# Performance work log

Measured on AMD Instinct MI355X. Metric: run time of the kernel, lower is better.

## Reference

```python
import jax, jax.numpy as jnp
import numpy as np

N, S, E, H = 4, 4096, 1024, 16
D = E // H  # 64


def setup_inputs() -> dict:
    key = jax.random.key(0)
    ks = jax.random.split(key, 6)
    scale = 0.02
    x = jax.random.normal(ks[0], (N, S, E), dtype=jnp.float32)
    Wq = jax.random.normal(ks[1], (E, E), dtype=jnp.float32) * scale
    Wk = jax.random.normal(ks[2], (E, E), dtype=jnp.float32) * scale
    Wv = jax.random.normal(ks[3], (E, E), dtype=jnp.float32) * scale
    Wo = jax.random.normal(ks[4], (E, E), dtype=jnp.float32) * scale
    bo = jax.random.normal(ks[5], (E,), dtype=jnp.float32) * scale
    return {"x": x, "Wq": Wq, "Wk": Wk, "Wv": Wv, "Wo": Wo, "bo": bo}


def reference(x, Wq, Wk, Wv, Wo, bo):
    n, s, _ = x.shape
    # torch nn.Linear(bias=False): y = x @ W.T  (W stored as [out, in])
    q = (x @ Wq.T).reshape(n, s, H, D).transpose(0, 2, 1, 3)  # (N, H, S, D)
    k = (x @ Wk.T).reshape(n, s, H, D).transpose(0, 2, 1, 3)  # (N, H, S, D)
    v = (x @ Wv.T).reshape(n, s, H, D).transpose(0, 2, 1, 3)  # (N, H, S, D)
    # Faithful to source: einsum subscripts applied to the PERMUTED (N,H,S,D)
    # tensors, so label q->H, h->S. energy: (N, H, H, S)
    energy = jnp.einsum('nqhd,nkhd->nqkh', q, k)
    attention = jax.nn.softmax(energy / (D ** 0.5), axis=3)
    # 'nqkh,nvhd->nqhd': k and v are independently summed free indices
    out = jnp.einsum('nqkh,nvhd->nqhd', attention, v).reshape(n, s, E)  # (N,S,E)
    return out @ Wo.T + bo
```

## Files before the change

kernel.cpp:

```cpp
#include <hip/hip_runtime.h>
#include <stdint.h>

typedef unsigned short u16;
typedef unsigned int   u32;
typedef __attribute__((ext_vector_type(8))) short short8;
typedef __attribute__((ext_vector_type(4))) float f32x4;
typedef __attribute__((ext_vector_type(8))) u16   u16x8;
typedef __attribute__((ext_vector_type(4))) u16   u16x4;

static constexpr size_t NX = (size_t)4 * 4096 * 1024;
static constexpr size_t NW = (size_t)1024 * 1024;

static constexpr size_t OFF_XB   = 0;
static constexpr size_t OFF_EN   = 0;
static constexpr size_t OFF_QK   = 33554432;
static constexpr size_t OFF_WQB  = 100663296;
static constexpr size_t OFF_WKB  = 102760448;
static constexpr size_t OFF_WOB  = 104857600;
static constexpr size_t OFF_WVST = 106954752;
static constexpr size_t OFF_VS   = 107216896;
static constexpr size_t OFF_GMAX = 111411200;
static constexpr size_t OFF_INVZ = 111415296;
static constexpr size_t OFF_ST   = 111419392;

static __device__ __forceinline__ u16 f2bf(float f) {
    u32 u = __builtin_bit_cast(u32, f);
    u += 0x7fffu + ((u >> 16) & 1u);
    return (u16)(u >> 16);
}
static __device__ __forceinline__ float bf2f(u16 v) {
    u32 u = ((u32)v) << 16;
    return __builtin_bit_cast(float, u);
}

#if __has_builtin(__builtin_amdgcn_global_load_lds)
#define HAVE_GLOAD_LDS 1
static __device__ __forceinline__ void gload_lds16(const void* g, void* l) {
    __builtin_amdgcn_global_load_lds(
        (__attribute__((address_space(1))) void*)(uintptr_t)g,
        (__attribute__((address_space(3))) void*)(uintptr_t)l,
        16, 0, 0);
}
#endif

#if __has_builtin(__builtin_amdgcn_sched_barrier)
#define SCHED_FENCE() __builtin_amdgcn_sched_barrier(0)
#else
#define SCHED_FENCE()
#endif

__global__ __launch_bounds__(256)
void cvt_kernel(const float* __restrict__ x, const float* __restrict__ wq,
                const float* __restrict__ wk, const float* __restrict__ wo,
                u16* __restrict__ xb, u16* __restrict__ wqb,
                u16* __restrict__ wkb, u16* __restrict__ wob)
{
    size_t i = ((size_t)blockIdx.x * 256 + threadIdx.x) * 8;
    const float* s; u16* dst; size_t o;
    if (i < NX) { s = x; dst = xb; o = i; }
    else {
        size_t r = i - NX;
        int w = (int)(r >> 20);
        o = r & (NW - 1);
        s   = (w == 0) ? wq  : (w == 1) ? wk  : wo;
        dst = (w == 0) ? wqb : (w == 1) ? wkb : wob;
    }
    f32x4 a = *(const f32x4*)&s[o];
    f32x4 c = *(const f32x4*)&s[o + 4];
    u16x8 v;
    v[0]=f2bf(a[0]); v[1]=f2bf(a[1]); v[2]=f2bf(a[2]); v[3]=f2bf(a[3]);
    v[4]=f2bf(c[0]); v[5]=f2bf(c[1]); v[6]=f2bf(c[2]); v[7]=f2bf(c[3]);
    *(u16x8*)&dst[o] = v;
}

__global__ __launch_bounds__(256)
void wvst_kernel(const float* __restrict__ Wv, u16* __restrict__ Bvs)
{
    int idx = blockIdx.x * 256 + threadIdx.x;
    int d = idx >> 10;
    int e = idx & 1023;
    float s = 0.f;
    #pragma unroll
    for (int h = 0; h < 16; ++h) s += Wv[(size_t)(h * 64 + d) * 1024 + e];
    Bvs[(size_t)d * 1024 + e] = f2bf(s);
}

__global__ __launch_bounds__(512, 2)
void gemm_qk(const u16* __restrict__ A, const u16* __restrict__ Bw,
             u16* __restrict__ C, int M, int N, int K, int lognbx)
{
    __shared__ u16 lds[65536];
    const int tid  = threadIdx.x;
    const int wave = tid >> 6;
    const int lane = tid & 63;

    const int nwg = gridDim.x;
    const int swz = ((int)blockIdx.x & 7) * (nwg >> 3) + ((int)blockIdx.x >> 3);
    const long col0 = (long)(swz & ((1 << lognbx) - 1)) * 256;
    const long row0 = (long)(swz >> lognbx) * 256;

    const int wr2 = wave >> 2;
    const int wc2 = wave & 3;
    const int fr  = lane & 15;
    const int kq  = lane >> 4;
    const int rxor = fr & 7;

    const int t255  = tid & 255;
    const int halfA = tid >> 8;
    const int gAsrc = (t255 & 7) ^ ((t255 >> 3) & 7);
    const u16* sA = A + (size_t)(row0 + halfA * 128 + (t255 >> 3)) * K + gAsrc * 8;
    const int dA = halfA * 8192 + t255 * 8;

    const int u  = (tid & 127) | ((tid >> 1) & 128);
    const int bh = (tid >> 7) & 1;
    const int gBsrc = (u & 7) ^ ((u >> 3) & 7);
    const u16* sB = Bw + (size_t)(col0 + bh * 128 + (u >> 3)) * K + gBsrc * 8;
    const int dB = bh * 8192 + u * 8;

    auto STAGE = [&](int buf, int k0) {
        #pragma unroll
        for (int l = 0; l < 4; ++l) {
#ifdef HAVE_GLOAD_LDS
            gload_lds16(sA + (size_t)l * 32 * K + k0, &lds[buf * 16384 + dA + l * 2048]);
            gload_lds16(sB + (size_t)l * 32 * K + k0, &lds[32768 + buf * 16384 + dB + l * 2048]);
#else
            *(short8*)&lds[buf * 16384 + dA + l * 2048] =
                *(const short8*)(sA + (size_t)l * 32 * K + k0);
            *(short8*)&lds[32768 + buf * 16384 + dB + l * 2048] =
                *(const short8*)(sB + (size_t)l * 32 * K + k0);
#endif
        }
    };

    f32x4 acc[8][4] = {};

    STAGE(0, 0);
    __syncthreads();

    const int nt = K >> 6;
    for (int t = 0; t < nt; ++t) {
        const int cur = t & 1;
        const int base  = cur * 16384;
        const int bbase = 32768 + cur * 16384;

        if (t + 1 < nt) STAGE(cur ^ 1, (t + 1) << 6);

        short8 af[4][2], ag[4][2], bf[2][2], bg[2][2];
        #pragma unroll
        for (int m = 0; m < 4; ++m) {
            const int row = wr2 * 128 + m * 16 + fr;
            #pragma unroll
            for (int kk = 0; kk < 2; ++kk)
                af[m][kk] = *(const short8*)&lds[base + row * 64 + (((kk << 2) | kq) ^ rxor) * 8];
        }
        #pragma unroll
        for (int n = 0; n < 2; ++n) {
            const int col = wc2 * 64 + n * 16 + fr;
            #pragma unroll
            for (int kk = 0; kk < 2; ++kk)
                bf[n][kk] = *(const short8*)&lds[bbase + col * 64 + (((kk << 2) | kq) ^ rxor) * 8];
        }
        #pragma unroll
        for (int m = 0; m < 4; ++m) {
            const int row = wr2 * 128 + 64 + m * 16 + fr;
            #pragma unroll
            for (int kk = 0; kk < 2; ++kk)
                ag[m][kk] = *(const short8*)&lds[base + row * 64 + (((kk << 2) | kq) ^ rxor) * 8];
        }
        SCHED_FENCE();

        __builtin_amdgcn_s_setprio(1);
        #pragma unroll
        for (int kk = 0; kk < 2; ++kk)
            #pragma unroll
            for (int m = 0; m < 4; ++m)
                #pragma unroll
                for (int n = 0; n < 2; ++n)
                    acc[m][n] = __builtin_amdgcn_mfma_f32_16x16x32_bf16(af[m][kk], bf[n][kk], acc[m][n], 0, 0, 0);
        __builtin_amdgcn_s_setprio(0);

        #pragma unroll
        for (int n = 0; n < 2; ++n) {
            const int col = wc2 * 64 + (n + 2) * 16 + fr;
            #pragma unroll
            for (int kk = 0; kk < 2; ++kk)
                bg[n][kk] = *(const short8*)&lds[bbase + col * 64 + (((kk << 2) | kq) ^ rxor) * 8];
        }
        SCHED_FENCE();

        __builtin_amdgcn_s_setprio(1);
        #pragma unroll
        for (int kk = 0; kk < 2; ++kk)
            #pragma unroll
            for (int m = 0; m < 4; ++m)
                #pragma unroll
                for (int n = 0; n < 2; ++n)
                    acc[m + 4][n] = __builtin_amdgcn_mfma_f32_16x16x32_bf16(ag[m][kk], bf[n][kk], acc[m + 4][n], 0, 0, 0);
        #pragma unroll
        for (int kk = 0; kk < 2; ++kk)
            #pragma unroll
            for (int m = 0; m < 4; ++m)
                #pragma unroll
                for (int n = 0; n < 2; ++n)
                    acc[m][n + 2] = __builtin_amdgcn_mfma_f32_16x16x32_bf16(af[m][kk], bg[n][kk], acc[m][n + 2], 0, 0, 0);
        #pragma unroll
        for (int kk = 0; kk < 2; ++kk)
            #pragma unroll
            for (int m = 0; m < 4; ++m)
                #pragma unroll
                for (int n = 0; n < 2; ++n)
                    acc[m + 4][n + 2] = __builtin_amdgcn_mfma_f32_16x16x32_bf16(ag[m][kk], bg[n][kk], acc[m + 4][n + 2], 0, 0, 0);
        __builtin_amdgcn_s_setprio(0);

        __syncthreads();
    }

    #pragma unroll
    for (int m = 0; m < 8; ++m) {
        #pragma unroll
        for (int n = 0; n < 4; ++n) {
            long gr = row0 + wr2 * 128 + m * 16 + kq * 4;
            long gc = col0 + wc2 * 64 + n * 16 + fr;
            #pragma unroll
            for (int j = 0; j < 4; ++j)
                C[(gr + j) * N + gc] = f2bf(acc[m][n][j]);
        }
    }
}

__global__ __launch_bounds__(256)
void gemm_vs(const u16* __restrict__ A, const u16* __restrict__ Bw,
             u16* __restrict__ C)
{
    __shared__ u16 lsA[2][64 * 32];
    __shared__ u16 lsB[2][64 * 32];
    const int tid  = threadIdx.x;
    const int wave = tid >> 6;
    const int lane = tid & 63;
    const long row0 = (long)blockIdx.x * 64;
    const int wr = (wave >> 1) * 32;
    const int wc = (wave & 1) * 32;
    const int fr = lane & 15;
    const int k8 = (lane >> 4) * 8;

    f32x4 acc[2][2] = {};
    const int c0 = tid;
    const u16* pa = &A [(row0 + (c0 >> 2)) * 1024 + (c0 & 3) * 8];
    const u16* pb = &Bw[((size_t)(c0 >> 2)) * 1024 + (c0 & 3) * 8];

    auto STAGE = [&](int buf, int k0) {
#ifdef HAVE_GLOAD_LDS
        gload_lds16(pa + k0, &lsA[buf][wave * 512]);
        gload_lds16(pb + k0, &lsB[buf][wave * 512]);
#else
        *(short8*)&lsA[buf][(size_t)c0 * 8] = *(const short8*)(pa + k0);
        *(short8*)&lsB[buf][(size_t)c0 * 8] = *(const short8*)(pb + k0);
#endif
    };

    STAGE(0, 0);
    __syncthreads();
    for (int t = 0; t < 32; ++t) {
        const int cur = t & 1;
        if (t + 1 < 32) STAGE(cur ^ 1, (t + 1) << 5);
        short8 af[2], bf[2];
        #pragma unroll
        for (int m = 0; m < 2; ++m)
            af[m] = *(const short8*)&lsA[cur][(wr + m * 16 + fr) * 32 + k8];
        #pragma unroll
        for (int n = 0; n < 2; ++n)
            bf[n] = *(const short8*)&lsB[cur][(wc + n * 16 + fr) * 32 + k8];
        #pragma unroll
        for (int m = 0; m < 2; ++m)
            #pragma unroll
            for (int n = 0; n < 2; ++n)
                acc[m][n] = __builtin_amdgcn_mfma_f32_16x16x32_bf16(af[m], bf[n], acc[m][n], 0, 0, 0);
        __syncthreads();
    }

    const int orow = (lane >> 4) * 4;
    #pragma unroll
    for (int m = 0; m < 2; ++m) {
        #pragma unroll
        for (int n = 0; n < 2; ++n) {
            long gr = row0 + wr + m * 16 + orow;
            int  gc = wc + n * 16 + fr;
            #pragma unroll
            for (int j = 0; j < 4; ++j)
                C[(gr + j) * 64 + gc] = f2bf(acc[m][n][j]);
        }
    }
}

__global__ __launch_bounds__(256)
void energy_kernel(const u16* __restrict__ QKb, float* __restrict__ E)
{
    const int lane = threadIdx.x & 63;
    const size_t site = (size_t)blockIdx.x * 4 + (threadIdx.x >> 6);
    const u16* qrow = QKb + site * 2048;
    const int hh = lane & 15;
    const int kg = (lane >> 4) * 8;
    short8 a0 = *(const short8*)&qrow[hh * 64 + kg];
    short8 a1 = *(const short8*)&qrow[hh * 64 + 32 + kg];
    short8 b0 = *(const short8*)&qrow[1024 + hh * 64 + kg];
    short8 b1 = *(const short8*)&qrow[1024 + hh * 64 + 32 + kg];
    f32x4 acc = {};
    acc = __builtin_amdgcn_mfma_f32_16x16x32_bf16(a0, b0, acc, 0, 0, 0);
    acc = __builtin_amdgcn_mfma_f32_16x16x32_bf16(a1, b1, acc, 0, 0, 0);
    float* out = E + site * 256;
    const int ib = (lane >> 4) * 4;
    #pragma unroll
    for (int r = 0; r < 4; ++r)
        out[(ib + r) * 16 + hh] = acc[r];
}

__global__ __launch_bounds__(256)
void stats_part(const float* __restrict__ E, float* __restrict__ pmax,
                float* __restrict__ psum)
{
    const int b = blockIdx.x, p = threadIdx.x;
    const float* e = E + (size_t)b * 64 * 256 + p;
    float m = -3.4e38f;
    float buf[64];
    #pragma unroll 8
    for (int s = 0; s < 64; ++s) {
        float v = e[(size_t)s * 256];
        buf[s] = v;
        m = fmaxf(m, v);
    }
    float z = 0.f;
    #pragma unroll 8
    for (int s = 0; s < 64; ++s) z += __expf((buf[s] - m) * 0.125f);
    pmax[b * 256 + p] = m;
    psum[b * 256 + p] = z;
}
__global__ __launch_bounds__(256)
void stats_comb(const float* __restrict__ pmax, const float* __restrict__ psum,
                float* __restrict__ gmax, float* __restrict__ invZ)
{
    const int n = blockIdx.x, p = threadIdx.x;
    float m = -3.4e38f;
    #pragma unroll 8
    for (int c = 0; c < 64; ++c) m = fmaxf(m, pmax[(n * 64 + c) * 256 + p]);
    float z = 0.f;
    #pragma unroll 8
    for (int c = 0; c < 64; ++c)
        z += psum[(n * 64 + c) * 256 + p] * __expf((pmax[(n * 64 + c) * 256 + p] - m) * 0.125f);
    gmax[n * 256 + p] = m;
    invZ[n * 256 + p] = 1.0f / z;
}

__global__ __launch_bounds__(256)
void g_kernel(const u16* __restrict__ Vsb, const u16* __restrict__ Wob,
              u16* __restrict__ G)
{
    __shared__ u16 lA[64 * 64];
    __shared__ u16 lB[256 * 64];
    const int tid = threadIdx.x;
    const int wave = tid >> 6, lane = tid & 63;
    const int op = blockIdx.x, uc = blockIdx.y, sl = blockIdx.z;

    {
        const int j = tid >> 2;
        const size_t srow = (size_t)16 * (64 * uc + j) + sl;
        #pragma unroll
        for (int h = 0; h < 2; ++h) {
            const int g = (tid & 3) + h * 4;
            u16x8 v = *(const u16x8*)&Vsb[srow * 64 + g * 8];
            *(u16x8*)&lA[j * 64 + ((g ^ (j & 7)) * 8)] = v;
        }
    }
    {
        const size_t o = (size_t)op * 256 + tid;
        #pragma unroll
        for (int g = 0; g < 8; ++g) {
            u16x8 v = *(const u16x8*)&Wob[o * 1024 + 64 * sl + g * 8];
            *(u16x8*)&lB[tid * 64 + ((g ^ (tid & 7)) * 8)] = v;
        }
    }
    __syncthreads();

    const int fr = lane & 15, kq = lane >> 4;
    f32x4 acc[4][4] = {};
    #pragma unroll
    for (int kk = 0; kk < 2; ++kk) {
        short8 af[4], bq[4];
        #pragma unroll
        for (int m = 0; m < 4; ++m) {
            const int j = m * 16 + fr;
            af[m] = *(const short8*)&lA[j * 64 + (((kq + 4 * kk) ^ (j & 7)) * 8)];
        }
        #pragma unroll
        for (int n = 0; n < 4; ++n) {
            const int o = wave * 64 + n * 16 + fr;
            bq[n] = *(const short8*)&lB[o * 64 + (((kq + 4 * kk) ^ (o & 7)) * 8)];
        }
        #pragma unroll
        for (int m = 0; m < 4; ++m)
            #pragma unroll
            for (int n = 0; n < 4; ++n)
                acc[m][n] = __builtin_amdgcn_mfma_f32_16x16x32_bf16(af[m], bq[n], acc[m][n], 0, 0, 0);
    }

    #pragma unroll
    for (int m = 0; m < 4; ++m) {
        #pragma unroll
        for (int n = 0; n < 4; ++n) {
            const int ocol = op * 256 + wave * 64 + n * 16 + fr;
            #pragma unroll
            for (int jj = 0; jj < 4; ++jj) {
                const int j = m * 16 + kq * 4 + jj;
                G[((size_t)16 * (64 * uc + j) + sl) * 1024 + ocol] = f2bf(acc[m][n][jj]);
            }
        }
    }
}

__global__ __launch_bounds__(256)
void comb_kernel(const float* __restrict__ En, const float* __restrict__ gmax,
                 const float* __restrict__ invZ, const u16* __restrict__ G,
                 const float* __restrict__ bo, float* __restrict__ out)
{
    __shared__ float sm[256], sz[256], sa[256];
    const int b = blockIdx.x;
    const int n = b >> 8, c = b & 255;
    const int t = threadIdx.x;
    sm[t] = gmax[n * 256 + t];
    sz[t] = invZ[n * 256 + t];
    __syncthreads();
    {
        const int sl = t >> 4, i = t & 15;
        const float* e = En + ((size_t)n * 4096 + c * 16 + sl) * 256 + i * 16;
        float a = 0.f;
        #pragma unroll
        for (int j = 0; j < 16; ++j)
            a += __expf((e[j] - sm[i * 16 + j]) * 0.125f) * sz[i * 16 + j];
        sa[sl * 16 + i] = a;
    }
    __syncthreads();

    const int o0 = t * 4;
    const u16* gp = G + ((size_t)n * 4096 + c * 16) * 1024 + o0;
    f32x4 g[16];
    #pragma unroll
    for (int sl = 0; sl < 16; ++sl) {
        u16x4 gv = *(const u16x4*)&gp[(size_t)sl * 1024];
        g[sl][0] = bf2f(gv[0]); g[sl][1] = bf2f(gv[1]);
        g[sl][2] = bf2f(gv[2]); g[sl][3] = bf2f(gv[3]);
    }
    const f32x4 b4 = *(const f32x4*)&bo[o0];
    #pragma unroll
    for (int i = 0; i < 16; ++i) {
        f32x4 acc = b4;
        #pragma unroll
        for (int sl = 0; sl < 16; ++sl) {
            const float a = sa[sl * 16 + i];
            acc[0] += a * g[sl][0];
            acc[1] += a * g[sl][1];
            acc[2] += a * g[sl][2];
            acc[3] += a * g[sl][3];
        }
        *(f32x4*)&out[((size_t)n * 4096 + i * 256 + c) * 1024 + o0] = acc;
    }
}

extern "C" void kernel_launch(void* const* d_in, const int* in_sizes, int n_in,
                              void* d_out, int out_size, void* d_ws, size_t ws_size,
                              hipStream_t stream)
{
    const float* x  = (const float*)d_in[0];
    const float* Wq = (const float*)d_in[1];
    const float* Wk = (const float*)d_in[2];
    const float* Wv = (const float*)d_in[3];
    const float* Wo = (const float*)d_in[4];
    const float* bo = (const float*)d_in[5];
    float* out = (float*)d_out;
    char* ws = (char*)d_ws;

    u16*   xb   = (u16*)  (ws + OFF_XB);
    float* En   = (float*)(ws + OFF_EN);
    u16*   QKb  = (u16*)  (ws + OFF_QK);
    u16*   G    = (u16*)  (ws + OFF_QK);
    u16*   Wqb  = (u16*)  (ws + OFF_WQB);
    u16*   Wkb  = (u16*)  (ws + OFF_WKB);
    u16*   Wob  = (u16*)  (ws + OFF_WOB);
    u16*   Bvs  = (u16*)  (ws + OFF_WVST);
    u16*   Vsb  = (u16*)  (ws + OFF_VS);
    float* gmax = (float*)(ws + OFF_GMAX);
    float* invZ = (float*)(ws + OFF_INVZ);
    float* pmax = (float*)(ws + OFF_ST);
    float* psum = (float*)(ws + OFF_ST + 262144);

    cvt_kernel <<<9728, 256, 0, stream>>>(x, Wq, Wk, Wo, xb, Wqb, Wkb, Wob);
    wvst_kernel<<<256,  256, 0, stream>>>(Wv, Bvs);

    gemm_qk<<<512, 512, 0, stream>>>(xb, Wqb, QKb, 16384, 2048, 1024, 3);
    gemm_vs<<<256, 256, 0, stream>>>(xb, Bvs, Vsb);

    energy_kernel<<<4096, 256, 0, stream>>>(QKb, En);

    stats_part<<<256, 256, 0, stream>>>(En, pmax, psum);
    stats_comb<<<4,   256, 0, stream>>>(pmax, psum, gmax, invZ);

    g_kernel<<<dim3(4, 16, 16), 256, 0, stream>>>(Vsb, Wob, G);

    comb_kernel<<<1024, 256, 0, stream>>>(En, gmax, invZ, G, bo, out);
}
```

Before: 179.7 us.

## Split QK GEMM staging into half-tile loads with interleaved barriers and manual waitcnt

Reworks the gemm_qk main loop so global-to-LDS staging is split into per-half A and B loads spread across four MFMA phases. A is prefetched two K-steps ahead and B one step ahead, with explicit vmcnt/lgkmcnt waits and raw s_barrier instead of a full __syncthreads per iteration. The aim is to overlap memory traffic with MFMA work in a finer-grained, HipKittens-style 8-wave schedule. It adds many barriers and relies on exact vmcnt accounting, so a miscount could cause races or stalls.

```diff
diff --git a/kernel.cpp b/kernel.cpp
--- a/kernel.cpp
+++ b/kernel.cpp
@@ -48,6 +48,10 @@
 #else
 #define SCHED_FENCE()
 #endif
+#define SBAR()   __builtin_amdgcn_s_barrier()
+#define VMCNT4() do { asm volatile("s_waitcnt vmcnt(4)" ::: "memory"); } while (0)
+#define VMCNT0() do { asm volatile("s_waitcnt vmcnt(0)" ::: "memory"); } while (0)
+#define LGKM0()  do { asm volatile("s_waitcnt lgkmcnt(0)" ::: "memory"); } while (0)
 
 __global__ __launch_bounds__(256)
 void cvt_kernel(const float* __restrict__ x, const float* __restrict__ wq,
@@ -103,72 +107,70 @@
     const int wc2 = wave & 3;
     const int fr  = lane & 15;
     const int kq  = lane >> 4;
-    const int rxor = fr & 7;
-
-    const int t255  = tid & 255;
-    const int halfA = tid >> 8;
-    const int gAsrc = (t255 & 7) ^ ((t255 >> 3) & 7);
-    const u16* sA = A + (size_t)(row0 + halfA * 128 + (t255 >> 3)) * K + gAsrc * 8;
-    const int dA = halfA * 8192 + t255 * 8;
-
-    const int u  = (tid & 127) | ((tid >> 1) & 128);
-    const int bh = (tid >> 7) & 1;
-    const int gBsrc = (u & 7) ^ ((u >> 3) & 7);
-    const u16* sB = Bw + (size_t)(col0 + bh * 128 + (u >> 3)) * K + gBsrc * 8;
-    const int dB = bh * 8192 + u * 8;
-
-    auto STAGE = [&](int buf, int k0) {
-        #pragma unroll
-        for (int l = 0; l < 4; ++l) {
+    const int rx  = fr & 7;
+
+    const u16* Abase = A  + row0 * K;
+    const u16* Bbase = Bw + col0 * K;
+
+    auto STAGE_A = [&](int t, int h) {
+        u16* slot = &lds[(((t & 1) << 1) | h) << 13];
+        const u16* src = Abase + (size_t)(h * 128) * K + ((size_t)t << 6);
+        #pragma unroll
+        for (int l = 0; l < 2; ++l) {
+            const int G = wave * 128 + l * 64 + lane;
+            const int rr = G >> 3;
+            const int gs = (G & 7) ^ (rr & 7);
 #ifdef HAVE_GLOAD_LDS
-            gload_lds16(sA + (size_t)l * 32 * K + k0, &lds[buf * 16384 + dA + l * 2048]);
-            gload_lds16(sB + (size_t)l * 32 * K + k0, &lds[32768 + buf * 16384 + dB + l * 2048]);
+            gload_lds16(src + (size_t)rr * K + gs * 8, slot + wave * 1024 + l * 512);
 #else
-            *(short8*)&lds[buf * 16384 + dA + l * 2048] =
-                *(const short8*)(sA + (size_t)l * 32 * K + k0);
-            *(short8*)&lds[32768 + buf * 16384 + dB + l * 2048] =
-                *(const short8*)(sB + (size_t)l * 32 * K + k0);
+            *(short8*)&slot[G * 8] = *(const short8*)(src + (size_t)rr * K + gs * 8);
 #endif
         }
     };
+    auto STAGE_B = [&](int t, int h) {
+        u16* slot = &lds[32768 + ((((t & 1) << 1) | h) << 13)];
+        const u16* src = Bbase + (size_t)(h * 128) * K + ((size_t)t << 6);
+        #pragma unroll
+        for (int l = 0; l < 2; ++l) {
+            const int G = wave * 128 + l * 64 + lane;
+            const int rr = G >> 3;
+            const int gs = (G & 7) ^ (rr & 7);
+#ifdef HAVE_GLOAD_LDS
+            gload_lds16(src + (size_t)rr * K + gs * 8, slot + wave * 1024 + l * 512);
+#else
+            *(short8*)&slot[G * 8] = *(const short8*)(src + (size_t)rr * K + gs * 8);
+#endif
+        }
+    };
+
+    auto LDA = [&](int t, int m, int kk) -> short8 {
+        const u16* slot = &lds[(((t & 1) << 1) | wr2) << 13];
+        const int rr = m * 16 + fr;
+        return *(const short8*)&slot[rr * 64 + ((((kk << 2) | kq)) ^ rx) * 8];
+    };
+    auto LDB = [&](int t, int n, int kk) -> short8 {
+        const u16* slot = &lds[32768 + ((((t & 1) << 1) | (wc2 >> 1)) << 13)];
+        const int rr = (wc2 & 1) * 64 + n * 16 + fr;
+        return *(const short8*)&slot[rr * 64 + ((((kk << 2) | kq)) ^ rx) * 8];
+    };
 
     f32x4 acc[8][4] = {};
-
-    STAGE(0, 0);
-    __syncthreads();
+    short8 af03[4][2], af47[4][2], bf01[2][2], bf23[2][2];
+
+    STAGE_A(0, 0); STAGE_A(0, 1); STAGE_B(0, 0); STAGE_B(0, 1);
+    STAGE_A(1, 0); STAGE_A(1, 1);
+    VMCNT4();
+    SBAR();
 
     const int nt = K >> 6;
     for (int t = 0; t < nt; ++t) {
-        const int cur = t & 1;
-        const int base  = cur * 16384;
-        const int bbase = 32768 + cur * 16384;
-
-        if (t + 1 < nt) STAGE(cur ^ 1, (t + 1) << 6);
-
-        short8 af[4][2], ag[4][2], bf[2][2], bg[2][2];
-        #pragma unroll
-        for (int m = 0; m < 4; ++m) {
-            const int row = wr2 * 128 + m * 16 + fr;
-            #pragma unroll
-            for (int kk = 0; kk < 2; ++kk)
-                af[m][kk] = *(const short8*)&lds[base + row * 64 + (((kk << 2) | kq) ^ rxor) * 8];
-        }
-        #pragma unroll
-        for (int n = 0; n < 2; ++n) {
-            const int col = wc2 * 64 + n * 16 + fr;
-            #pragma unroll
-            for (int kk = 0; kk < 2; ++kk)
-                bf[n][kk] = *(const short8*)&lds[bbase + col * 64 + (((kk << 2) | kq) ^ rxor) * 8];
-        }
-        #pragma unroll
-        for (int m = 0; m < 4; ++m) {
-            const int row = wr2 * 128 + 64 + m * 16 + fr;
-            #pragma unroll
-            for (int kk = 0; kk < 2; ++kk)
-                ag[m][kk] = *(const short8*)&lds[base + row * 64 + (((kk << 2) | kq) ^ rxor) * 8];
-        }
-        SCHED_FENCE();
-
+        #pragma unroll
+        for (int m = 0; m < 4; ++m) { af03[m][0] = LDA(t, m, 0); af03[m][1] = LDA(t, m, 1); }
+        #pragma unroll
+        for (int n = 0; n < 2; ++n) { bf01[n][0] = LDB(t, n, 0); bf01[n][1] = LDB(t, n, 1); }
+        if (t + 1 < nt) STAGE_B(t + 1, 0);
+        SBAR();
+        LGKM0(); SCHED_FENCE();
         __builtin_amdgcn_s_setprio(1);
         #pragma unroll
         for (int kk = 0; kk < 2; ++kk)
@@ -176,18 +178,17 @@
             for (int m = 0; m < 4; ++m)
                 #pragma unroll
                 for (int n = 0; n < 2; ++n)
-                    acc[m][n] = __builtin_amdgcn_mfma_f32_16x16x32_bf16(af[m][kk], bf[n][kk], acc[m][n], 0, 0, 0);
+                    acc[m][n] = __builtin_amdgcn_mfma_f32_16x16x32_bf16(af03[m][kk], bf01[n][kk], acc[m][n], 0, 0, 0);
         __builtin_amdgcn_s_setprio(0);
-
-        #pragma unroll
-        for (int n = 0; n < 2; ++n) {
-            const int col = wc2 * 64 + (n + 2) * 16 + fr;
-            #pragma unroll
-            for (int kk = 0; kk < 2; ++kk)
-                bg[n][kk] = *(const short8*)&lds[bbase + col * 64 + (((kk << 2) | kq) ^ rxor) * 8];
-        }
-        SCHED_FENCE();
-
+        SBAR();
+
+        #pragma unroll
+        for (int m = 0; m < 4; ++m) { af47[m][0] = LDA(t, m + 4, 0); af47[m][1] = LDA(t, m + 4, 1); }
+        #pragma unroll
+        for (int n = 0; n < 2; ++n) { bf23[n][0] = LDB(t, n + 2, 0); bf23[n][1] = LDB(t, n + 2, 1); }
+        if (t + 1 < nt) STAGE_B(t + 1, 1);
+        SBAR();
+        LGKM0(); SCHED_FENCE();
         __builtin_amdgcn_s_setprio(1);
         #pragma unroll
         for (int kk = 0; kk < 2; ++kk)
@@ -195,24 +196,40 @@
             for (int m = 0; m < 4; ++m)
                 #pragma unroll
                 for (int n = 0; n < 2; ++n)
-                    acc[m + 4][n] = __builtin_amdgcn_mfma_f32_16x16x32_bf16(ag[m][kk], bf[n][kk], acc[m + 4][n], 0, 0, 0);
+                    acc[m][n + 2] = __builtin_amdgcn_mfma_f32_16x16x32_bf16(af03[m][kk], bf23[n][kk], acc[m][n + 2], 0, 0, 0);
+        __builtin_amdgcn_s_setprio(0);
+        SBAR();
+
+        if (t + 2 < nt) STAGE_A(t + 2, 0);
+        SBAR();
+        __builtin_amdgcn_s_setprio(1);
         #pragma unroll
         for (int kk = 0; kk < 2; ++kk)
             #pragma unroll
             for (int m = 0; m < 4; ++m)
                 #pragma unroll
                 for (int n = 0; n < 2; ++n)
-                    acc[m][n + 2] = __builtin_amdgcn_mfma_f32_16x16x32_bf16(af[m][kk], bg[n][kk], acc[m][n + 2], 0, 0, 0);
+                    acc[m + 4][n] = __builtin_amdgcn_mfma_f32_16x16x32_bf16(af47[m][kk], bf01[n][kk], acc[m + 4][n], 0, 0, 0);
+        __builtin_amdgcn_s_setprio(0);
+        SBAR();
+
+        if (t + 2 < nt) {
+            STAGE_A(t + 2, 1);
+            VMCNT4();
+        } else if (t + 1 < nt) {
+            VMCNT0();
+        }
+        SBAR();
+        __builtin_amdgcn_s_setprio(1);
         #pragma unroll
         for (int kk = 0; kk < 2; ++kk)
             #pragma unroll
             for (int m = 0; m < 4; ++m)
                 #pragma unroll
                 for (int n = 0; n < 2; ++n)
-                    acc[m + 4][n + 2] = __builtin_amdgcn_mfma_f32_16x16x32_bf16(ag[m][kk], bg[n][kk], acc[m + 4][n + 2], 0, 0, 0);
+                    acc[m + 4][n + 2] = __builtin_amdgcn_mfma_f32_16x16x32_bf16(af47[m][kk], bf23[n][kk], acc[m + 4][n + 2], 0, 0, 0);
         __builtin_amdgcn_s_setprio(0);
-
-        __syncthreads();
+        SBAR();
     }
 
     #pragma unroll
```

Result: slower. 187.6 us (+4.3%).

## Shrink QK GEMM tile to 256x128 with K-step 32 and online-softmax stats

Applied to the files above, without the earlier changes.

The QK projection GEMM moves from a 256x256 tile with K-step 64 to a 256x128 tile with K-step 32. That cuts LDS from 128KB to 48KB per block and the accumulators from 32 to 16 per wave, and raises occupancy from 2 to 4 blocks per CU, with twice as many workgroups. The cost is lower arithmetic intensity per tile, twice as many barrier iterations, and the loss of the interleaved LDS-load/MFMA schedule. The stats_part kernel switches to a single-pass online max/sum, dropping the 64-float register buffer at the cost of an extra exp per element.

```diff
diff --git a/kernel.cpp b/kernel.cpp
--- a/kernel.cpp
+++ b/kernel.cpp
@@ -85,142 +85,83 @@
     Bvs[(size_t)d * 1024 + e] = f2bf(s);
 }
 
-__global__ __launch_bounds__(512, 2)
+__global__ __launch_bounds__(512, 4)
 void gemm_qk(const u16* __restrict__ A, const u16* __restrict__ Bw,
              u16* __restrict__ C, int M, int N, int K, int lognbx)
 {
-    __shared__ u16 lds[65536];
+    __shared__ u16 lsA[2][256 * 32];
+    __shared__ u16 lsB[2][128 * 32];
     const int tid  = threadIdx.x;
     const int wave = tid >> 6;
     const int lane = tid & 63;
 
     const int nwg = gridDim.x;
     const int swz = ((int)blockIdx.x & 7) * (nwg >> 3) + ((int)blockIdx.x >> 3);
-    const long col0 = (long)(swz & ((1 << lognbx) - 1)) * 256;
+    const long col0 = (long)(swz & ((1 << lognbx) - 1)) * 128;
     const long row0 = (long)(swz >> lognbx) * 256;
 
-    const int wr2 = wave >> 2;
-    const int wc2 = wave & 3;
-    const int fr  = lane & 15;
-    const int kq  = lane >> 4;
-    const int rxor = fr & 7;
-
-    const int t255  = tid & 255;
-    const int halfA = tid >> 8;
-    const int gAsrc = (t255 & 7) ^ ((t255 >> 3) & 7);
-    const u16* sA = A + (size_t)(row0 + halfA * 128 + (t255 >> 3)) * K + gAsrc * 8;
-    const int dA = halfA * 8192 + t255 * 8;
-
-    const int u  = (tid & 127) | ((tid >> 1) & 128);
-    const int bh = (tid >> 7) & 1;
-    const int gBsrc = (u & 7) ^ ((u >> 3) & 7);
-    const u16* sB = Bw + (size_t)(col0 + bh * 128 + (u >> 3)) * K + gBsrc * 8;
-    const int dB = bh * 8192 + u * 8;
+    const int wr = (wave >> 1) * 64;
+    const int wc = (wave & 1) * 64;
+    const int fr = lane & 15;
+    const int kq = lane >> 4;
+    const int rx = fr & 3;
+
+    const int GA0 = tid, GA1 = tid + 512;
+    const int rA0 = GA0 >> 2, gA0 = (GA0 & 3) ^ (rA0 & 3);
+    const int rA1 = GA1 >> 2, gA1 = (GA1 & 3) ^ (rA1 & 3);
+    const int rB  = tid >> 2, gB  = (tid & 3) ^ (rB & 3);
+    const u16* pa0 = A  + (size_t)(row0 + rA0) * K + gA0 * 8;
+    const u16* pa1 = A  + (size_t)(row0 + rA1) * K + gA1 * 8;
+    const u16* pb  = Bw + (size_t)(col0 + rB ) * K + gB  * 8;
 
     auto STAGE = [&](int buf, int k0) {
-        #pragma unroll
-        for (int l = 0; l < 4; ++l) {
 #ifdef HAVE_GLOAD_LDS
-            gload_lds16(sA + (size_t)l * 32 * K + k0, &lds[buf * 16384 + dA + l * 2048]);
-            gload_lds16(sB + (size_t)l * 32 * K + k0, &lds[32768 + buf * 16384 + dB + l * 2048]);
+        gload_lds16(pa0 + k0, &lsA[buf][wave * 512]);
+        gload_lds16(pa1 + k0, &lsA[buf][4096 + wave * 512]);
+        gload_lds16(pb  + k0, &lsB[buf][wave * 512]);
 #else
-            *(short8*)&lds[buf * 16384 + dA + l * 2048] =
-                *(const short8*)(sA + (size_t)l * 32 * K + k0);
-            *(short8*)&lds[32768 + buf * 16384 + dB + l * 2048] =
-                *(const short8*)(sB + (size_t)l * 32 * K + k0);
+        *(short8*)&lsA[buf][(size_t)GA0 * 8] = *(const short8*)(pa0 + k0);
+        *(short8*)&lsA[buf][(size_t)GA1 * 8] = *(const short8*)(pa1 + k0);
+        *(short8*)&lsB[buf][(size_t)tid * 8] = *(const short8*)(pb  + k0);
 #endif
-        }
     };
 
-    f32x4 acc[8][4] = {};
+    f32x4 acc[4][4] = {};
 
     STAGE(0, 0);
     __syncthreads();
 
-    const int nt = K >> 6;
+    const int nt = K >> 5;
     for (int t = 0; t < nt; ++t) {
         const int cur = t & 1;
-        const int base  = cur * 16384;
-        const int bbase = 32768 + cur * 16384;
-
-        if (t + 1 < nt) STAGE(cur ^ 1, (t + 1) << 6);
-
-        short8 af[4][2], ag[4][2], bf[2][2], bg[2][2];
-        #pragma unroll
-        for (int m = 0; m < 4; ++m) {
-            const int row = wr2 * 128 + m * 16 + fr;
-            #pragma unroll
-            for (int kk = 0; kk < 2; ++kk)
-                af[m][kk] = *(const short8*)&lds[base + row * 64 + (((kk << 2) | kq) ^ rxor) * 8];
-        }
-        #pragma unroll
-        for (int n = 0; n < 2; ++n) {
-            const int col = wc2 * 64 + n * 16 + fr;
-            #pragma unroll
-            for (int kk = 0; kk < 2; ++kk)
-                bf[n][kk] = *(const short8*)&lds[bbase + col * 64 + (((kk << 2) | kq) ^ rxor) * 8];
-        }
-        #pragma unroll
-        for (int m = 0; m < 4; ++m) {
-            const int row = wr2 * 128 + 64 + m * 16 + fr;
-            #pragma unroll
-            for (int kk = 0; kk < 2; ++kk)
-                ag[m][kk] = *(const short8*)&lds[base + row * 64 + (((kk << 2) | kq) ^ rxor) * 8];
-        }
+        if (t + 1 < nt) STAGE(cur ^ 1, (t + 1) << 5);
+
+        short8 af[4], bf[4];
+        #pragma unroll
+        for (int m = 0; m < 4; ++m)
+            af[m] = *(const short8*)&lsA[cur][(wr + m * 16 + fr) * 32 + ((kq ^ rx) * 8)];
+        #pragma unroll
+        for (int n = 0; n < 4; ++n)
+            bf[n] = *(const short8*)&lsB[cur][(wc + n * 16 + fr) * 32 + ((kq ^ rx) * 8)];
         SCHED_FENCE();
 
         __builtin_amdgcn_s_setprio(1);
         #pragma unroll
-        for (int kk = 0; kk < 2; ++kk)
-            #pragma unroll
-            for (int m = 0; m < 4; ++m)
-                #pragma unroll
-                for (int n = 0; n < 2; ++n)
-                    acc[m][n] = __builtin_amdgcn_mfma_f32_16x16x32_bf16(af[m][kk], bf[n][kk], acc[m][n], 0, 0, 0);
+        for (int m = 0; m < 4; ++m)
+            #pragma unroll
+            for (int n = 0; n < 4; ++n)
+                acc[m][n] = __builtin_amdgcn_mfma_f32_16x16x32_bf16(af[m], bf[n], acc[m][n], 0, 0, 0);
         __builtin_amdgcn_s_setprio(0);
 
-        #pragma unroll
-        for (int n = 0; n < 2; ++n) {
-            const int col = wc2 * 64 + (n + 2) * 16 + fr;
-            #pragma unroll
-            for (int kk = 0; kk < 2; ++kk)
-                bg[n][kk] = *(const short8*)&lds[bbase + col * 64 + (((kk << 2) | kq) ^ rxor) * 8];
-        }
-        SCHED_FENCE();
-
-        __builtin_amdgcn_s_setprio(1);
-        #pragma unroll
-        for (int kk = 0; kk < 2; ++kk)
-            #pragma unroll
-            for (int m = 0; m < 4; ++m)
-                #pragma unroll
-                for (int n = 0; n < 2; ++n)
-                    acc[m + 4][n] = __builtin_amdgcn_mfma_f32_16x16x32_bf16(ag[m][kk], bf[n][kk], acc[m + 4][n], 0, 0, 0);
-        #pragma unroll
-        for (int kk = 0; kk < 2; ++kk)
-            #pragma unroll
-            for (int m = 0; m < 4; ++m)
-                #pragma unroll
-                for (int n = 0; n < 2; ++n)
-                    acc[m][n + 2] = __builtin_amdgcn_mfma_f32_16x16x32_bf16(af[m][kk], bg[n][kk], acc[m][n + 2], 0, 0, 0);
-        #pragma unroll
-        for (int kk = 0; kk < 2; ++kk)
-            #pragma unroll
-            for (int m = 0; m < 4; ++m)
-                #pragma unroll
-                for (int n = 0; n < 2; ++n)
-                    acc[m + 4][n + 2] = __builtin_amdgcn_mfma_f32_16x16x32_bf16(ag[m][kk], bg[n][kk], acc[m + 4][n + 2], 0, 0, 0);
-        __builtin_amdgcn_s_setprio(0);
-
         __syncthreads();
     }
 
     #pragma unroll
-    for (int m = 0; m < 8; ++m) {
+    for (int m = 0; m < 4; ++m) {
         #pragma unroll
         for (int n = 0; n < 4; ++n) {
-            long gr = row0 + wr2 * 128 + m * 16 + kq * 4;
-            long gc = col0 + wc2 * 64 + n * 16 + fr;
+            long gr = row0 + wr + m * 16 + kq * 4;
+            long gc = col0 + wc + n * 16 + fr;
             #pragma unroll
             for (int j = 0; j < 4; ++j)
                 C[(gr + j) * N + gc] = f2bf(acc[m][n][j]);
@@ -320,17 +261,13 @@
 {
     const int b = blockIdx.x, p = threadIdx.x;
     const float* e = E + (size_t)b * 64 * 256 + p;
-    float m = -3.4e38f;
-    float buf[64];
-    #pragma unroll 8
+    float m = -3.4e38f, z = 0.f;
     for (int s = 0; s < 64; ++s) {
         float v = e[(size_t)s * 256];
-        buf[s] = v;
-        m = fmaxf(m, v);
-    }
-    float z = 0.f;
-    #pragma unroll 8
-    for (int s = 0; s < 64; ++s) z += __expf((buf[s] - m) * 0.125f);
+        float mn = fmaxf(m, v);
+        z = z * __expf((m - mn) * 0.125f) + __expf((v - mn) * 0.125f);
+        m = mn;
+    }
     pmax[b * 256 + p] = m;
     psum[b * 256 + p] = z;
 }
@@ -340,10 +277,8 @@
 {
     const int n = blockIdx.x, p = threadIdx.x;
     float m = -3.4e38f;
-    #pragma unroll 8
     for (int c = 0; c < 64; ++c) m = fmaxf(m, pmax[(n * 64 + c) * 256 + p]);
     float z = 0.f;
-    #pragma unroll 8
     for (int c = 0; c < 64; ++c)
         z += psum[(n * 64 + c) * 256 + p] * __expf((pmax[(n * 64 + c) * 256 + p] - m) * 0.125f);
     gmax[n * 256 + p] = m;
@@ -494,7 +429,7 @@
     cvt_kernel <<<9728, 256, 0, stream>>>(x, Wq, Wk, Wo, xb, Wqb, Wkb, Wob);
     wvst_kernel<<<256,  256, 0, stream>>>(Wv, Bvs);
 
-    gemm_qk<<<512, 512, 0, stream>>>(xb, Wqb, QKb, 16384, 2048, 1024, 3);
+    gemm_qk<<<1024, 512, 0, stream>>>(xb, Wqb, QKb, 16384, 2048, 1024, 4);
     gemm_vs<<<256, 256, 0, stream>>>(xb, Bvs, Vsb);
 
     energy_kernel<<<4096, 256, 0, stream>>>(QKb, En);
```

After: 177.4 us. Within noise of the previous version (-1.3%).

## Fuse energy computation with softmax partial stats and merge conversion kernels

Applied to the files above, without the earlier changes.

Merges the weight/input bf16 conversion and the Wv head-sum into one launch. Fuses the energy MFMA kernel with the per-chunk online max/sum statistics, so the energy tensor no longer has to be re-read by a separate stats pass. The stats are reduced across waves in shared memory. The trade-off is a smaller energy grid of 256 blocks, each looping over 16 sites, which lowers parallelism and adds exp work per element inside the loop.

```diff
diff --git a/kernel.cpp b/kernel.cpp
--- a/kernel.cpp
+++ b/kernel.cpp
@@ -50,39 +50,40 @@
 #endif
 
 __global__ __launch_bounds__(256)
-void cvt_kernel(const float* __restrict__ x, const float* __restrict__ wq,
-                const float* __restrict__ wk, const float* __restrict__ wo,
-                u16* __restrict__ xb, u16* __restrict__ wqb,
-                u16* __restrict__ wkb, u16* __restrict__ wob)
-{
-    size_t i = ((size_t)blockIdx.x * 256 + threadIdx.x) * 8;
-    const float* s; u16* dst; size_t o;
-    if (i < NX) { s = x; dst = xb; o = i; }
-    else {
-        size_t r = i - NX;
-        int w = (int)(r >> 20);
-        o = r & (NW - 1);
-        s   = (w == 0) ? wq  : (w == 1) ? wk  : wo;
-        dst = (w == 0) ? wqb : (w == 1) ? wkb : wob;
-    }
-    f32x4 a = *(const f32x4*)&s[o];
-    f32x4 c = *(const f32x4*)&s[o + 4];
-    u16x8 v;
-    v[0]=f2bf(a[0]); v[1]=f2bf(a[1]); v[2]=f2bf(a[2]); v[3]=f2bf(a[3]);
-    v[4]=f2bf(c[0]); v[5]=f2bf(c[1]); v[6]=f2bf(c[2]); v[7]=f2bf(c[3]);
-    *(u16x8*)&dst[o] = v;
-}
-
-__global__ __launch_bounds__(256)
-void wvst_kernel(const float* __restrict__ Wv, u16* __restrict__ Bvs)
-{
-    int idx = blockIdx.x * 256 + threadIdx.x;
-    int d = idx >> 10;
-    int e = idx & 1023;
-    float s = 0.f;
-    #pragma unroll
-    for (int h = 0; h < 16; ++h) s += Wv[(size_t)(h * 64 + d) * 1024 + e];
-    Bvs[(size_t)d * 1024 + e] = f2bf(s);
+void cvt_all_kernel(const float* __restrict__ x, const float* __restrict__ wq,
+                    const float* __restrict__ wk, const float* __restrict__ wv,
+                    const float* __restrict__ wo,
+                    u16* __restrict__ xb, u16* __restrict__ wqb,
+                    u16* __restrict__ wkb, u16* __restrict__ wob,
+                    u16* __restrict__ Bvs)
+{
+    const int blk = blockIdx.x;
+    if (blk < 9728) {
+        size_t i = ((size_t)blk * 256 + threadIdx.x) * 8;
+        const float* s; u16* dst; size_t o;
+        if (i < NX) { s = x; dst = xb; o = i; }
+        else {
+            size_t r = i - NX;
+            int w = (int)(r >> 20);
+            o = r & (NW - 1);
+            s   = (w == 0) ? wq  : (w == 1) ? wk  : wo;
+            dst = (w == 0) ? wqb : (w == 1) ? wkb : wob;
+        }
+        f32x4 a = *(const f32x4*)&s[o];
+        f32x4 c = *(const f32x4*)&s[o + 4];
+        u16x8 v;
+        v[0]=f2bf(a[0]); v[1]=f2bf(a[1]); v[2]=f2bf(a[2]); v[3]=f2bf(a[3]);
+        v[4]=f2bf(c[0]); v[5]=f2bf(c[1]); v[6]=f2bf(c[2]); v[7]=f2bf(c[3]);
+        *(u16x8*)&dst[o] = v;
+    } else {
+        int idx = (blk - 9728) * 256 + threadIdx.x;
+        int d = idx >> 10;
+        int e = idx & 1023;
+        float s = 0.f;
+        #pragma unroll
+        for (int h = 0; h < 16; ++h) s += wv[(size_t)(h * 64 + d) * 1024 + e];
+        Bvs[(size_t)d * 1024 + e] = f2bf(s);
+    }
 }
 
 __global__ __launch_bounds__(512, 2)
@@ -293,57 +294,63 @@
 }
 
 __global__ __launch_bounds__(256)
-void energy_kernel(const u16* __restrict__ QKb, float* __restrict__ E)
-{
-    const int lane = threadIdx.x & 63;
-    const size_t site = (size_t)blockIdx.x * 4 + (threadIdx.x >> 6);
-    const u16* qrow = QKb + site * 2048;
+void energy_stats_kernel(const u16* __restrict__ QKb, float* __restrict__ E,
+                         float* __restrict__ pmax, float* __restrict__ psum)
+{
+    __shared__ float red[4][64][8];
+    const int wave = threadIdx.x >> 6, lane = threadIdx.x & 63;
+    const size_t s0 = (size_t)blockIdx.x * 64 + wave * 16;
     const int hh = lane & 15;
-    const int kg = (lane >> 4) * 8;
-    short8 a0 = *(const short8*)&qrow[hh * 64 + kg];
-    short8 a1 = *(const short8*)&qrow[hh * 64 + 32 + kg];
-    short8 b0 = *(const short8*)&qrow[1024 + hh * 64 + kg];
-    short8 b1 = *(const short8*)&qrow[1024 + hh * 64 + 32 + kg];
-    f32x4 acc = {};
-    acc = __builtin_amdgcn_mfma_f32_16x16x32_bf16(a0, b0, acc, 0, 0, 0);
-    acc = __builtin_amdgcn_mfma_f32_16x16x32_bf16(a1, b1, acc, 0, 0, 0);
-    float* out = E + site * 256;
-    const int ib = (lane >> 4) * 4;
-    #pragma unroll
-    for (int r = 0; r < 4; ++r)
-        out[(ib + r) * 16 + hh] = acc[r];
-}
-
-__global__ __launch_bounds__(256)
-void stats_part(const float* __restrict__ E, float* __restrict__ pmax,
-                float* __restrict__ psum)
-{
-    const int b = blockIdx.x, p = threadIdx.x;
-    const float* e = E + (size_t)b * 64 * 256 + p;
-    float m = -3.4e38f;
-    float buf[64];
-    #pragma unroll 8
-    for (int s = 0; s < 64; ++s) {
-        float v = e[(size_t)s * 256];
-        buf[s] = v;
-        m = fmaxf(m, v);
-    }
-    float z = 0.f;
-    #pragma unroll 8
-    for (int s = 0; s < 64; ++s) z += __expf((buf[s] - m) * 0.125f);
-    pmax[b * 256 + p] = m;
-    psum[b * 256 + p] = z;
-}
+    const int kg = lane >> 4;
+    float m[4] = {-3.4e38f, -3.4e38f, -3.4e38f, -3.4e38f};
+    float z[4] = {0.f, 0.f, 0.f, 0.f};
+
+    for (int s = 0; s < 16; ++s) {
+        const u16* qrow = QKb + (s0 + s) * 2048;
+        short8 a0 = *(const short8*)&qrow[hh * 64 + kg * 8];
+        short8 a1 = *(const short8*)&qrow[hh * 64 + 32 + kg * 8];
+        short8 b0 = *(const short8*)&qrow[1024 + hh * 64 + kg * 8];
+        short8 b1 = *(const short8*)&qrow[1024 + hh * 64 + 32 + kg * 8];
+        f32x4 acc = {};
+        acc = __builtin_amdgcn_mfma_f32_16x16x32_bf16(a0, b0, acc, 0, 0, 0);
+        acc = __builtin_amdgcn_mfma_f32_16x16x32_bf16(a1, b1, acc, 0, 0, 0);
+        float* o = E + (s0 + s) * 256;
+        #pragma unroll
+        for (int r = 0; r < 4; ++r) {
+            const float v = acc[r];
+            o[(kg * 4 + r) * 16 + hh] = v;
+            const float mn = fmaxf(m[r], v);
+            z[r] = z[r] * __expf((m[r] - mn) * 0.125f) + __expf((v - mn) * 0.125f);
+            m[r] = mn;
+        }
+    }
+    #pragma unroll
+    for (int r = 0; r < 4; ++r) { red[wave][lane][r] = m[r]; red[wave][lane][4 + r] = z[r]; }
+    __syncthreads();
+
+    const int t = threadIdx.x;
+    const int i = t >> 4, j = t & 15;
+    const int ln = (i >> 2) * 16 + j, r = i & 3;
+    float M = -3.4e38f, Z = 0.f;
+    #pragma unroll
+    for (int w = 0; w < 4; ++w) {
+        const float mw = red[w][ln][r], zw = red[w][ln][4 + r];
+        const float mn = fmaxf(M, mw);
+        Z = Z * __expf((M - mn) * 0.125f) + zw * __expf((mw - mn) * 0.125f);
+        M = mn;
+    }
+    pmax[blockIdx.x * 256 + t] = M;
+    psum[blockIdx.x * 256 + t] = Z;
+}
+
 __global__ __launch_bounds__(256)
 void stats_comb(const float* __restrict__ pmax, const float* __restrict__ psum,
                 float* __restrict__ gmax, float* __restrict__ invZ)
 {
     const int n = blockIdx.x, p = threadIdx.x;
     float m = -3.4e38f;
-    #pragma unroll 8
     for (int c = 0; c < 64; ++c) m = fmaxf(m, pmax[(n * 64 + c) * 256 + p]);
     float z = 0.f;
-    #pragma unroll 8
     for (int c = 0; c < 64; ++c)
         z += psum[(n * 64 + c) * 256 + p] * __expf((pmax[(n * 64 + c) * 256 + p] - m) * 0.125f);
     gmax[n * 256 + p] = m;
@@ -491,16 +498,13 @@
     float* pmax = (float*)(ws + OFF_ST);
     float* psum = (float*)(ws + OFF_ST + 262144);
 
-    cvt_kernel <<<9728, 256, 0, stream>>>(x, Wq, Wk, Wo, xb, Wqb, Wkb, Wob);
-    wvst_kernel<<<256,  256, 0, stream>>>(Wv, Bvs);
+    cvt_all_kernel<<<9984, 256, 0, stream>>>(x, Wq, Wk, Wv, Wo, xb, Wqb, Wkb, Wob, Bvs);
 
     gemm_qk<<<512, 512, 0, stream>>>(xb, Wqb, QKb, 16384, 2048, 1024, 3);
     gemm_vs<<<256, 256, 0, stream>>>(xb, Bvs, Vsb);
 
-    energy_kernel<<<4096, 256, 0, stream>>>(QKb, En);
-
-    stats_part<<<256, 256, 0, stream>>>(En, pmax, psum);
-    stats_comb<<<4,   256, 0, stream>>>(pmax, psum, gmax, invZ);
+    energy_stats_kernel<<<256, 256, 0, stream>>>(QKb, En, pmax, psum);
+    stats_comb<<<4, 256, 0, stream>>>(pmax, psum, gmax, invZ);
 
     g_kernel<<<dim3(4, 16, 16), 256, 0, stream>>>(Vsb, Wob, G);
 
```

After: 171.9 us. 4.3% less time.
